# Kernel optimization log

Hardware: AMD Instinct MI355X
Metric: run time of the kernel (lower is better)

## Reference

```python
import jax, jax.numpy as jnp
import numpy as np

N_NODES = 10000
N_EDGES = 160000
N_GRAPHS = 16
IN_FEAT = 128
DIMS = [(128, 512), (512, 256), (256, 64), (64, 32)]


def _lin_params(key, fin, fout):
    w = jax.random.normal(key, (fin, fout), jnp.float32) * (1.0 / np.sqrt(fin))
    b = jnp.zeros((fout,), jnp.float32)
    return w, b


def setup_inputs() -> dict:
    key = jax.random.key(0)
    ks = jax.random.split(key, 64)
    inp = {}
    inp['x'] = jax.random.normal(ks[0], (N_NODES, IN_FEAT), jnp.float32)
    inp['edge_index'] = jax.random.randint(ks[1], (2, N_EDGES), 0, N_NODES, jnp.int64 if jax.config.jax_enable_x64 else jnp.int32)
    inp['batch'] = jnp.sort(jax.random.randint(ks[2], (N_NODES,), 0, N_GRAPHS))
    ki = 3
    for li, (fin, fout) in enumerate(DIMS, start=1):
        for nm in ['q', 'k', 'v', 's']:
            w, b = _lin_params(ks[ki], fin, fout); ki += 1
            inp[f'W{nm}{li}'] = w
            inp[f'b{nm}{li}'] = b
    inp['Wg'], inp['bg'] = _lin_params(ks[ki], 32, 1); ki += 1
    inp['Wf'], inp['bf'] = _lin_params(ks[ki], 32, 9)
    return inp


def _segment_softmax(logits, seg, num_segments):
    m = jax.ops.segment_max(logits, seg, num_segments=num_segments)
    e = jnp.exp(logits - m[seg])
    s = jax.ops.segment_sum(e, seg, num_segments=num_segments)
    return e / s[seg]


def _transformer_conv(x, src, dst, Wq, bq, Wk, bk, Wv, bv, Ws, bs):
    # PyG TransformerConv, heads=1: attention over incoming edges per dst node.
    n = x.shape[0]
    q = x @ Wq + bq
    k = x @ Wk + bk
    v = x @ Wv + bv
    d = q.shape[-1]
    logits = jnp.sum(q[dst] * k[src], axis=-1) / jnp.sqrt(jnp.asarray(d, x.dtype))
    alpha = _segment_softmax(logits, dst, n)  # [E]
    agg = jax.ops.segment_sum(alpha[:, None] * v[src], dst, num_segments=n)
    return agg + (x @ Ws + bs)  # root/skip connection


def reference(x, edge_index, batch,
              Wq1, bq1, Wk1, bk1, Wv1, bv1, Ws1, bs1,
              Wq2, bq2, Wk2, bk2, Wv2, bv2, Ws2, bs2,
              Wq3, bq3, Wk3, bk3, Wv3, bv3, Ws3, bs3,
              Wq4, bq4, Wk4, bk4, Wv4, bv4, Ws4, bs4,
              Wg, bg, Wf, bf):
    src, dst = edge_index[0], edge_index[1]
    layers = [
        (Wq1, bq1, Wk1, bk1, Wv1, bv1, Ws1, bs1),
        (Wq2, bq2, Wk2, bk2, Wv2, bv2, Ws2, bs2),
        (Wq3, bq3, Wk3, bk3, Wv3, bv3, Ws3, bs3),
        (Wq4, bq4, Wk4, bk4, Wv4, bv4, Ws4, bs4),
    ]
    h = x
    for p in layers:
        h = jax.nn.elu(_transformer_conv(h, src, dst, *p))
    # GlobalAttention pooling: gate softmax per graph, weighted sum.
    gate = (h @ Wg + bg)[:, 0]  # [N]
    a = _segment_softmax(gate, batch, N_GRAPHS)
    pooled = jax.ops.segment_sum(a[:, None] * h, batch, num_segments=N_GRAPHS)  # [G, 32]
    return pooled @ Wf + bf  # [G, 9]
```

## Files before the change

### kernel.cpp

```cpp
#include <hip/hip_runtime.h>
#include <hip/hip_bf16.h>
#include <math.h>


typedef __bf16 bf16x8 __attribute__((ext_vector_type(8)));
typedef __bf16 bf16x4 __attribute__((ext_vector_type(4)));
typedef __bf16 bf16x2 __attribute__((ext_vector_type(2)));
typedef float f32x4 __attribute__((ext_vector_type(4)));
typedef float f32x2 __attribute__((ext_vector_type(2)));

#define GBM 128
#define GBN 128
#define GBK 64

#if __has_builtin(__builtin_amdgcn_global_load_lds)
#define ASYNC_LDS 1
__device__ __forceinline__ void gload16(const __bf16* g, __bf16* l) {
  __builtin_amdgcn_global_load_lds(
      (const __attribute__((address_space(1))) unsigned int*)g,
      (__attribute__((address_space(3))) unsigned int*)l, 16, 0, 0);
}
#endif

#if __has_builtin(__builtin_amdgcn_fdot2_f32_bf16)
#define HAS_BF16_DOT2 1
#endif

__device__ __forceinline__ void xcd_swizzle(int& bx, int& by) {
  const int gx = gridDim.x;
  const int nwg = gx * gridDim.y;
  const int orig = blockIdx.y * gx + blockIdx.x;
  const int q = nwg >> 3, r = nwg & 7;
  const int xcd = orig & 7, ii = orig >> 3;
  const int wgid = (xcd < r ? xcd * (q + 1) : r * (q + 1) + (xcd - r) * q) + ii;
  bx = wgid % gx;
  by = wgid / gx;
}

__global__ __launch_bounds__(256) void gemm_mfma_kernel(
    const __bf16* __restrict__ A, const __bf16* __restrict__ Bt,
    const float* __restrict__ bias, __bf16* __restrict__ qkvs,
    int M, int K, int Nc) {
  __shared__ __bf16 As[GBM * 64];
  __shared__ __bf16 Bs[GBN * 64];
  const int tid = threadIdx.x;
  const int wave = tid >> 6;
  const int lane = tid & 63;
  const int quad = lane >> 4;
  const int l16 = lane & 15;
  int bx, by;
  xcd_swizzle(bx, by);
  const int m0 = by * GBM;
  const int n0 = bx * GBN;
  const int wm = (wave & 1) * 64;
  const int wn = (wave >> 1) * 64;

  const int r8 = lane >> 3;
  const int sseg = lane & 7;

  f32x4 acc[4][4] = {};

  for (int k0 = 0; k0 < K; k0 += GBK) {
#pragma unroll
    for (int it = 0; it < 4; ++it) {
      const int rbase = wave * 32 + it * 8;
      const int row = rbase + r8;
      const int sw = sseg ^ r8;
      const __bf16* ga = A + (size_t)(m0 + row) * K + k0 + sw * 8;
      const __bf16* gb = Bt + (size_t)(n0 + row) * K + k0 + sw * 8;
#ifdef ASYNC_LDS
      gload16(ga, As + rbase * 64);
      gload16(gb, Bs + rbase * 64);
#else
      *(bf16x8*)(As + row * 64 + sseg * 8) = *(const bf16x8*)ga;
      *(bf16x8*)(Bs + row * 64 + sseg * 8) = *(const bf16x8*)gb;
#endif
    }
    __syncthreads();

#pragma unroll
    for (int ks = 0; ks < 2; ++ks) {
      bf16x8 af[4], bfr[4];
#pragma unroll
      for (int i = 0; i < 4; ++i) {
        const int ra = wm + i * 16 + l16;
        const int rb = wn + i * 16 + l16;
        const int ps = ((ks * 4 + quad) ^ (l16 & 7)) * 8;
        af[i]  = *(const bf16x8*)(As + ra * 64 + ps);
        bfr[i] = *(const bf16x8*)(Bs + rb * 64 + ps);
      }
#pragma unroll
      for (int mi = 0; mi < 4; ++mi)
#pragma unroll
        for (int ni = 0; ni < 4; ++ni)
          acc[mi][ni] = __builtin_amdgcn_mfma_f32_16x16x32_bf16(
              af[mi], bfr[ni], acc[mi][ni], 0, 0, 0);
    }
    __syncthreads();
  }

  float bsv[4];
#pragma unroll
  for (int ni = 0; ni < 4; ++ni) bsv[ni] = bias[n0 + wn + ni * 16 + l16];
#pragma unroll
  for (int mi = 0; mi < 4; ++mi) {
#pragma unroll
    for (int r = 0; r < 4; ++r) {
      int row = m0 + wm + mi * 16 + quad * 4 + r;
      if (row < M) {
        size_t rb = (size_t)row * Nc;
#pragma unroll
        for (int ni = 0; ni < 4; ++ni) {
          int col = n0 + wn + ni * 16 + l16;
          qkvs[rb + col] = (__bf16)(acc[mi][ni][r] + bsv[ni]);
        }
      }
    }
  }
}

__global__ __launch_bounds__(256) void gemm_mfma_elu_kernel(
    const __bf16* __restrict__ A, const __bf16* __restrict__ Bt,
    const float* __restrict__ bias_s, const float* __restrict__ bias_v,
    const int* __restrict__ offs, __bf16* __restrict__ out,
    int M, int K, int Nc) {
  __shared__ __bf16 As[GBM * 64];
  __shared__ __bf16 Bs[GBN * 64];
  const int tid = threadIdx.x;
  const int wave = tid >> 6;
  const int lane = tid & 63;
  const int quad = lane >> 4;
  const int l16 = lane & 15;
  int bx, by;
  xcd_swizzle(bx, by);
  const int m0 = by * GBM;
  const int n0 = bx * GBN;
  const int wm = (wave & 1) * 64;
  const int wn = (wave >> 1) * 64;

  const int r8 = lane >> 3;
  const int sseg = lane & 7;

  f32x4 acc[4][4] = {};

  for (int k0 = 0; k0 < K; k0 += GBK) {
#pragma unroll
    for (int it = 0; it < 4; ++it) {
      const int rbase = wave * 32 + it * 8;
      const int row = rbase + r8;
      const int sw = sseg ^ r8;
      const __bf16* ga = A + (size_t)(m0 + row) * K + k0 + sw * 8;
      const __bf16* gb = Bt + (size_t)(n0 + row) * K + k0 + sw * 8;
#ifdef ASYNC_LDS
      gload16(ga, As + rbase * 64);
      gload16(gb, Bs + rbase * 64);
#else
      *(bf16x8*)(As + row * 64 + sseg * 8) = *(const bf16x8*)ga;
      *(bf16x8*)(Bs + row * 64 + sseg * 8) = *(const bf16x8*)gb;
#endif
    }
    __syncthreads();

#pragma unroll
    for (int ks = 0; ks < 2; ++ks) {
      bf16x8 af[4], bfr[4];
#pragma unroll
      for (int i = 0; i < 4; ++i) {
        const int ra = wm + i * 16 + l16;
        const int rb = wn + i * 16 + l16;
        const int ps = ((ks * 4 + quad) ^ (l16 & 7)) * 8;
        af[i]  = *(const bf16x8*)(As + ra * 64 + ps);
        bfr[i] = *(const bf16x8*)(Bs + rb * 64 + ps);
      }
#pragma unroll
      for (int mi = 0; mi < 4; ++mi)
#pragma unroll
        for (int ni = 0; ni < 4; ++ni)
          acc[mi][ni] = __builtin_amdgcn_mfma_f32_16x16x32_bf16(
              af[mi], bfr[ni], acc[mi][ni], 0, 0, 0);
    }
    __syncthreads();
  }

  float bsv[4], bvv[4];
#pragma unroll
  for (int ni = 0; ni < 4; ++ni) {
    const int col = n0 + wn + ni * 16 + l16;
    bsv[ni] = bias_s[col];
    bvv[ni] = bias_v[col];
  }
#pragma unroll
  for (int mi = 0; mi < 4; ++mi) {
#pragma unroll
    for (int r = 0; r < 4; ++r) {
      int row = m0 + wm + mi * 16 + quad * 4 + r;
      if (row < M) {
        const float bm = (offs[row + 1] - offs[row]) > 0 ? 1.f : 0.f;
        size_t rb = (size_t)row * Nc;
#pragma unroll
        for (int ni = 0; ni < 4; ++ni) {
          int col = n0 + wn + ni * 16 + l16;
          float v = acc[mi][ni][r] + bsv[ni] + bm * bvv[ni];
          v = (v > 0.f) ? v : expm1f(v);
          out[rb + col] = (__bf16)v;
        }
      }
    }
  }
}

#define NTILES 180
#define BTOT 3456
#define XTOT 320000
#define ABT_T 65536
#define UB_T 512
__global__ __launch_bounds__(256) void setup_pack_kernel(
    const float* W1q, const float* W1k, const float* W1v, const float* W1s,
    const float* W2q, const float* W2k, const float* W2v, const float* W2s,
    const float* W3q, const float* W3k, const float* W3v, const float* W3s,
    const float* W0v, const float* W0s,
    __bf16* __restrict__ Wt, __bf16* __restrict__ Bt2,
    const float* b0q, const float* b0k, const float* b0v, const float* b0s,
    const float* b1q, const float* b1k, const float* b1v, const float* b1s,
    const float* b2q, const float* b2k, const float* b2v, const float* b2s,
    const float* b3q, const float* b3k, const float* b3v, const float* b3s,
    const float* W0q, const float* W0k,
    const float* __restrict__ x, __bf16* __restrict__ xb,
    float* __restrict__ bcat,
    const int* __restrict__ dst, int* __restrict__ deg, int E,
    __bf16* __restrict__ Abt, float* __restrict__ biasu) {
  __shared__ float tile[64][65];
  const int tid = threadIdx.x;

  if (blockIdx.x < NTILES) {
    const int tb = blockIdx.x;
    const float* src;
    __bf16* dst_;
    int K, F, RS, CO, k0, j0;
    if (tb < 128) {
      const int m = tb >> 5, t = tb & 31;
      const float* Ws[4] = {W1q, W1k, W1v, W1s};
      src = Ws[m]; K = 512; F = 256; RS = 512; CO = 0;
      k0 = (t & 7) * 64; j0 = (t >> 3) * 64;
      dst_ = Wt + 262144 + (size_t)m * 131072;
    } else if (tb < 144) {
      const int u = tb - 128, m = u >> 2;
      const float* Ws[4] = {W2q, W2k, W2v, W2s};
      src = Ws[m]; K = 256; F = 64; RS = 256; CO = 0;
      k0 = (u & 3) * 64; j0 = 0;
      dst_ = Wt + 786432 + (size_t)m * 16384;
    } else if (tb < 148) {
      const int m = tb - 144;
      const float* Ws[4] = {W3q, W3k, W3v, W3s};
      src = Ws[m]; K = 64; F = 32; RS = 64; CO = 0;
      k0 = 0; j0 = 0;
      dst_ = Wt + 851968 + (size_t)m * 2048;
    } else {
      const int u = tb - 148, m = u >> 4, t = u & 15;
      src = m ? W0s : W0v; K = 128; F = 512; RS = 256; CO = m * 128;
      k0 = (t & 1) * 64; j0 = (t >> 1) * 64;
      dst_ = Bt2;
    }

    const int lj = tid & 63;
    const int lr = tid >> 6;
#pragma unroll
    for (int it = 0; it < 16; ++it) {
      const int kr = it * 4 + lr;
      float v = 0.f;
      if (k0 + kr < K && j0 + lj < F) v = src[(size_t)(k0 + kr) * F + j0 + lj];
      tile[kr][lj] = v;
    }
    __syncthreads();
#pragma unroll
    for (int it = 0; it < 16; ++it) {
      const int jr = it * 4 + lr;
      if (j0 + jr < F && k0 + lj < K)
        dst_[(size_t)(j0 + jr) * RS + CO + k0 + lj] = (__bf16)tile[lj][jr];
    }
    return;
  }

  const int t = (blockIdx.x - NTILES) * 256 + tid;
  if (t < XTOT) {
    float4 v = ((const float4*)x)[t];
    bf16x4 o;
    o[0] = (__bf16)v.x; o[1] = (__bf16)v.y; o[2] = (__bf16)v.z; o[3] = (__bf16)v.w;
    *(bf16x4*)(xb + (size_t)t * 4) = o;
  } else if (t < XTOT + BTOT) {
    int u = t - XTOT;
    int l, local, fsh, boff;
    if (u < 2048)      { l = 0; local = u;        fsh = 9; boff = 0; }
    else if (u < 3072) { l = 1; local = u - 2048; fsh = 8; boff = 2048; }
    else if (u < 3328) { l = 2; local = u - 3072; fsh = 6; boff = 3072; }
    else               { l = 3; local = u - 3328; fsh = 5; boff = 3328; }
    const int fout = 1 << fsh;
    int blk = local >> fsh, j = local & (fout - 1);
    const float* b;
    if (l == 0)      b = blk == 0 ? b0q : blk == 1 ? b0k : blk == 2 ? b0v : b0s;
    else if (l == 1) b = blk == 0 ? b1q : blk == 1 ? b1k : blk == 2 ? b1v : b1s;
    else if (l == 2) b = blk == 0 ? b2q : blk == 1 ? b2k : blk == 2 ? b2v : b2s;
    else             b = blk == 0 ? b3q : blk == 1 ? b3k : blk == 2 ? b3v : b3s;
    bcat[boff + local] = b[j];
  } else if (t < XTOT + BTOT + E) {
    int e = t - (XTOT + BTOT);
    atomicAdd(&deg[dst[e]], 1);
  } else if (t < XTOT + BTOT + E + ABT_T) {
    const int u = t - (XTOT + BTOT + E);
    const int n = u >> 9;
    const int rem = u & 511;
    const int k = rem >> 2;
    const int q = rem & 3;
    const float4* wq = (const float4*)(W0q + (size_t)k * 512) + q * 32;
    const float4* wk = (const float4*)(W0k + (size_t)n * 512) + q * 32;
    float sacc = 0.f;
#pragma unroll 4
    for (int jj = 0; jj < 32; ++jj) {
      float4 a = wq[jj], b = wk[jj];
      sacc += a.x * b.x + a.y * b.y + a.z * b.z + a.w * b.w;
    }
    sacc += __shfl_xor(sacc, 1);
    sacc += __shfl_xor(sacc, 2);
    if (q == 0) Abt[(size_t)n * 128 + k] = (__bf16)sacc;
  } else if (t < XTOT + BTOT + E + ABT_T + UB_T) {
    const int u = t - (XTOT + BTOT + E + ABT_T);
    const int n = u >> 2;
    const int q = u & 3;
    const float4* wk = (const float4*)(W0k + (size_t)n * 512) + q * 32;
    const float4* bq = (const float4*)b0q + q * 32;
    float sacc = 0.f;
#pragma unroll 4
    for (int jj = 0; jj < 32; ++jj) {
      float4 a = wk[jj], b = bq[jj];
      sacc += a.x * b.x + a.y * b.y + a.z * b.z + a.w * b.w;
    }
    sacc += __shfl_xor(sacc, 1);
    sacc += __shfl_xor(sacc, 2);
    if (q == 0) biasu[n] = sacc;
  }
}

__global__ __launch_bounds__(1024) void scan_kernel(const int* __restrict__ deg,
                                                    int* __restrict__ offs, int N) {
  __shared__ int sums[1024];
  const int tid = threadIdx.x;
  const int chunk = (N + 1023) / 1024;
  const int start = tid * chunk;
  int s = 0;
  for (int i = 0; i < chunk; ++i) {
    int idx = start + i;
    if (idx < N) s += deg[idx];
  }
  sums[tid] = s;
  __syncthreads();
  for (int off = 1; off < 1024; off <<= 1) {
    int t = (tid >= off) ? sums[tid - off] : 0;
    __syncthreads();
    sums[tid] += t;
    __syncthreads();
  }
  int run = (tid == 0) ? 0 : sums[tid - 1];
  for (int i = 0; i < chunk; ++i) {
    int idx = start + i;
    if (idx < N) {
      offs[idx] = run;
      run += deg[idx];
    }
  }
  if (tid == 1023) offs[N] = sums[1023];
}

__global__ void scatter_kernel(const int* __restrict__ src, const int* __restrict__ dst,
                               const int* __restrict__ offs, int* __restrict__ cursor,
                               int* __restrict__ csr_src, int E) {
  int e = blockIdx.x * blockDim.x + threadIdx.x;
  if (e >= E) return;
  int d = dst[e];
  int pos = offs[d] + atomicAdd(&cursor[d], 1);
  csr_src[pos] = src[e];
}

template <int D, int LPG_LOG2, bool GATE>
__global__ __launch_bounds__(256) void attn_fused_kernel(
    const __bf16* __restrict__ qkvs, const int* __restrict__ csr_src,
    const int* __restrict__ offs, __bf16* __restrict__ h_out, int N,
    float scale, const float* __restrict__ Wg, const float* __restrict__ bg,
    float* __restrict__ gate_out) {
  constexpr int LPG = 1 << LPG_LOG2;
  constexpr int NG = 64 / LPG;
  constexpr int NIT = D / (8 * LPG);
  constexpr int LD = 4 * D;
  const int node = (blockIdx.x * 256 + threadIdx.x) >> 6;
  const int lane = threadIdx.x & 63;
  if (node >= N) return;
  const int g = lane >> LPG_LOG2;
  const int l = lane & (LPG - 1);
  const int begin = offs[node];
  const int deg = offs[node + 1] - begin;

  const __bf16* qrow = qkvs + (size_t)node * LD;
  bf16x8 qreg[NIT];
#pragma unroll
  for (int it = 0; it < NIT; ++it)
    qreg[it] = *(const bf16x8*)(qrow + it * LPG * 8 + l * 8);

  float m0 = 0.f;
  float s = 0.f;
  f32x2 acc[NIT][4] = {};

  bf16x8 kA[NIT], vA[NIT], kB[NIT], vB[NIT];

  auto load_rows = [&](bool valid, int idx, bf16x8 (&kv)[NIT], bf16x8 (&vv)[NIT]) {
    const int sidx = valid ? csr_src[begin + idx] : 0;
    const __bf16* kr = qkvs + (size_t)sidx * LD + D + l * 8;
    if (valid) {
#pragma unroll
      for (int it = 0; it < NIT; ++it) {
        kv[it] = *(const bf16x8*)(kr + it * LPG * 8);
        vv[it] = *(const bf16x8*)(kr + D + it * LPG * 8);
      }
    }
  };

  auto compute = [&](bool valid, bool first, const bf16x8 (&kv)[NIT],
                     const bf16x8 (&vv)[NIT]) {
    float p = 0.f;
// ... 68 lines not shown

  if (g == 0) {
    float rr[NIT][8];
#pragma unroll
    for (int it = 0; it < NIT; ++it) {
      const int f0 = it * LPG * 8 + l * 8;
      bf16x8 sk = *(const bf16x8*)(qrow + 3 * D + f0);
      bf16x8 o;
#pragma unroll
      for (int j2 = 0; j2 < 4; ++j2) {
        float r0 = acc[it][j2][0] * inv + (float)sk[2 * j2];
        float r1 = acc[it][j2][1] * inv + (float)sk[2 * j2 + 1];
        r0 = (r0 > 0.f) ? r0 : expm1f(r0);
        r1 = (r1 > 0.f) ? r1 : expm1f(r1);
        rr[it][2 * j2] = r0;
        rr[it][2 * j2 + 1] = r1;
        o[2 * j2] = (__bf16)r0;
        o[2 * j2 + 1] = (__bf16)r1;
      }
      *(bf16x8*)(h_out + (size_t)node * D + f0) = o;
    }
    if (GATE) {
      float gp = 0.f;
#pragma unroll
      for (int j = 0; j < 8; ++j) gp += rr[0][j] * Wg[l * 8 + j];
#pragma unroll
      for (int off = 1; off < LPG; off <<= 1) gp += __shfl_xor(gp, off);
      if (l == 0) gate_out[node] = gp + bg[0];
    }
  }
}

template <int LPG_LOG2>
__global__ __launch_bounds__(256) void attn_lin_kernel(
    const __bf16* __restrict__ u, const __bf16* __restrict__ hsrc,
    const int* __restrict__ csr_src, const int* __restrict__ offs,
    __bf16* __restrict__ buf, int N, float scale) {
  constexpr int D = 128;
  constexpr int LPG = 1 << LPG_LOG2;
  constexpr int NG = 64 / LPG;
  constexpr int NIT = D / (8 * LPG);
  const int node = (blockIdx.x * 256 + threadIdx.x) >> 6;
  const int lane = threadIdx.x & 63;
  if (node >= N) return;
  const int g = lane >> LPG_LOG2;
  const int l = lane & (LPG - 1);
  const int begin = offs[node];
  const int deg = offs[node + 1] - begin;

  const __bf16* urow = u + (size_t)node * D;
  bf16x8 qreg[NIT];
#pragma unroll
  for (int it = 0; it < NIT; ++it)
    qreg[it] = *(const bf16x8*)(urow + it * LPG * 8 + l * 8);

  float m0 = 0.f;
  float s = 0.f;
  f32x2 acc[NIT][4] = {};

  bf16x8 kA[NIT], kB[NIT];

  auto load_rows = [&](bool valid, int idx, bf16x8 (&kv)[NIT]) {
    const int sidx = valid ? csr_src[begin + idx] : 0;
    const __bf16* hr = hsrc + (size_t)sidx * D + l * 8;
    if (valid) {
#pragma unroll
      for (int it = 0; it < NIT; ++it)
        kv[it] = *(const bf16x8*)(hr + it * LPG * 8);
    }
  };

  auto compute = [&](bool valid, bool first, const bf16x8 (&kv)[NIT]) {
    float p = 0.f;
    if (valid) {
#ifdef HAS_BF16_DOT2
#pragma unroll
// ... 50 lines not shown
    compute(valB, false, kB);
  }

#pragma unroll
  for (int off = LPG; off < 64; off <<= 1) {
    s += __shfl_xor(s, off);
#pragma unroll
    for (int it = 0; it < NIT; ++it)
#pragma unroll
      for (int j2 = 0; j2 < 4; ++j2) {
        acc[it][j2][0] += __shfl_xor(acc[it][j2][0], off);
        acc[it][j2][1] += __shfl_xor(acc[it][j2][1], off);
      }
  }
  const float inv = (deg > 0) ? (1.0f / s) : 0.f;

  if (g == 0) {
#pragma unroll
    for (int it = 0; it < NIT; ++it) {
      const int f0 = it * LPG * 8 + l * 8;
      bf16x8 o;
#pragma unroll
      for (int j2 = 0; j2 < 4; ++j2) {
        o[2 * j2]     = (__bf16)(acc[it][j2][0] * inv);
        o[2 * j2 + 1] = (__bf16)(acc[it][j2][1] * inv);
      }
      *(bf16x8*)(buf + (size_t)node * 256 + f0) = o;
      *(bf16x8*)(buf + (size_t)node * 256 + 128 + f0) =
          *(const bf16x8*)(hsrc + (size_t)node * D + f0);
    }
  }
}

__global__ __launch_bounds__(256) void pool_final_kernel(
    const __bf16* __restrict__ h, const float* __restrict__ gate,
    const int* __restrict__ batch, int N, const float* __restrict__ Wf,
    const float* __restrict__ bf_, float* __restrict__ out) {
  __shared__ float red[256];
  __shared__ float pooled_s[32];
  __shared__ float m_s, inv_s;
  __shared__ int sb[2];
  const int g = blockIdx.x;
  const int tid = threadIdx.x;

  if (tid < 2) {
    int target = g + tid;
    int lo = 0, hi = N;
    while (lo < hi) {
      int mid = (lo + hi) >> 1;
      if (batch[mid] < target) lo = mid + 1;
      else hi = mid;
    }
    sb[tid] = lo;
  }
  __syncthreads();
  const int s = sb[0];
  const int e_end = sb[1];

  float m = -INFINITY;
  for (int i = s + tid; i < e_end; i += 256) m = fmaxf(m, gate[i]);
  red[tid] = m;
  __syncthreads();
  for (int off = 128; off; off >>= 1) {
    if (tid < off) red[tid] = fmaxf(red[tid], red[tid + off]);
    __syncthreads();
  }
  if (tid == 0) m_s = red[0];
  __syncthreads();
  m = m_s;

  float ss = 0.f;
  for (int i = s + tid; i < e_end; i += 256) ss += __expf(gate[i] - m);
  red[tid] = ss;
  __syncthreads();
  for (int off = 128; off; off >>= 1) {
    if (tid < off) red[tid] += red[tid + off];
    __syncthreads();
  }
  if (tid == 0) inv_s = (e_end > s) ? (1.0f / red[0]) : 0.f;
  __syncthreads();
  const float inv = inv_s;

  const int f = tid & 31;
  const int grp = tid >> 5;
  float acc = 0.f;
  for (int i = s + grp; i < e_end; i += 8)
    acc += __expf(gate[i] - m) * (float)h[(size_t)i * 32 + f];
  red[tid] = acc;
  __syncthreads();
  if (tid < 32) {
    float a = 0.f;
#pragma unroll
    for (int j = 0; j < 8; ++j) a += red[j * 32 + tid];
    pooled_s[tid] = a * inv;
  }
  __syncthreads();

  if (tid < 9) {
    float o = bf_[tid];
#pragma unroll
    for (int kk = 0; kk < 32; ++kk) o += pooled_s[kk] * Wf[kk * 9 + tid];
    out[g * 9 + tid] = o;
  }
}

#define WTOT 860160
#define ATOT 16384
#define UBTOT 128
#define B2TOT 131072
extern "C" void kernel_launch(void* const* d_in, const int* in_sizes, int n_in,
                              void* d_out, int out_size, void* d_ws, size_t ws_size,
                              hipStream_t stream) {
  const int N = in_sizes[2];
  const int E = in_sizes[1] / 2;
  const int G = 16;
  const int NP = N + 128;

  const float* x = (const float*)d_in[0];
  const int* ei = (const int*)d_in[1];
  const int* batch = (const int*)d_in[2];
  const int* src = ei;
  const int* dst = ei + E;
  const float* Wg = (const float*)d_in[35];
  const float* bg = (const float*)d_in[36];
  const float* Wf = (const float*)d_in[37];
  const float* bf_ = (const float*)d_in[38];
  float* out = (float*)d_out;

  char* p = (char*)d_ws;
  auto carve = [&](size_t bytes) -> char* {
    char* r = p;
    p += (bytes + 255) & ~(size_t)255;
    return r;
  };
  int* deg = (int*)carve((size_t)2 * N * 4);
  int* cursor = deg + N;
  int* offs = (int*)carve((size_t)(N + 1) * 4);
  int* csr_src = (int*)carve((size_t)E * 4);
  __bf16* Ab = (__bf16*)carve((size_t)NP * 128 * 2);
  __bf16* Wt = (__bf16*)carve((size_t)WTOT * 2);
  float* bcat = (float*)carve(BTOT * 4);
  __bf16* qkvs = (__bf16*)carve((size_t)NP * 1024 * 2);
  __bf16* ha = (__bf16*)carve((size_t)NP * 512 * 2);
  __bf16* hb = (__bf16*)carve((size_t)NP * 512 * 2);
  float* gate = (float*)carve((size_t)N * 4);
  __bf16* ubuf = (__bf16*)carve((size_t)NP * 128 * 2);
  __bf16* cat = (__bf16*)carve((size_t)NP * 256 * 2);
  __bf16* Abt = (__bf16*)carve((size_t)ATOT * 2);
  float* biasu = (float*)carve((size_t)UBTOT * 4);
  __bf16* Bt2 = (__bf16*)carve((size_t)B2TOT * 2);
  (void)ws_size;

  hipMemsetAsync(deg, 0, (size_t)2 * N * 4, stream);
  const float** di = (const float**)d_in;
  const int miscb = (XTOT + BTOT + E + ABT_T + UB_T + 255) / 256;
  setup_pack_kernel<<<NTILES + miscb, 256, 0, stream>>>(
      di[11], di[13], di[15], di[17],
      di[19], di[21], di[23], di[25],
      di[27], di[29], di[31], di[33],
      di[7], di[9],
      Wt, Bt2,
      di[4], di[6], di[8], di[10],
      di[12], di[14], di[16], di[18],
      di[20], di[22], di[24], di[26],
      di[28], di[30], di[32], di[34],
      di[3], di[5],
      x, Ab, bcat, dst, deg, E, Abt, biasu);
  scan_kernel<<<1, 1024, 0, stream>>>(deg, offs, N);
  scatter_kernel<<<(E + 255) / 256, 256, 0, stream>>>(src, dst, offs, cursor, csr_src, E);

  const int agrid = ((size_t)N * 64 + 255) / 256;
  const int mg = (N + GBM - 1) / GBM;

  {
    dim3 g1(1, mg);
    gemm_mfma_kernel<<<g1, 256, 0, stream>>>(Ab, Abt, biasu, ubuf, N, 128, 128);
    attn_lin_kernel<3><<<agrid, 256, 0, stream>>>(ubuf, Ab, csr_src, offs, cat, N,
                                                  1.0f / sqrtf(512.f));
    dim3 g2(4, mg);
    gemm_mfma_elu_kernel<<<g2, 256, 0, stream>>>(cat, Bt2, di[10], di[8], offs,
                                                 ha, N, 256, 512);
  }

  const int fins[3] = {512, 256, 64};
  const int fouts[3] = {256, 64, 32};
  const size_t woffs[3] = {262144, 786432, 851968};
  const int boffs[3] = {2048, 3072, 3328};
  const __bf16* hin = ha;
  __bf16* houts[3] = {hb, ha, hb};

  for (int l = 0; l < 3; ++l) {
    const int fin = fins[l], fout = fouts[l];
    const int Nc = 4 * fout;
    __bf16* hout = houts[l];

    dim3 grid(Nc / GBN, mg);
    gemm_mfma_kernel<<<grid, 256, 0, stream>>>(hin, Wt + woffs[l], bcat + boffs[l],
                                               qkvs, N, fin, Nc);

    float scale = 1.0f / sqrtf((float)fout);
    if (l == 0) {
      attn_fused_kernel<256, 4, false><<<agrid, 256, 0, stream>>>(
          qkvs, csr_src, offs, hout, N, scale, nullptr, nullptr, nullptr);
    } else if (l == 1) {
      attn_fused_kernel<64, 3, false><<<agrid, 256, 0, stream>>>(
          qkvs, csr_src, offs, hout, N, scale, nullptr, nullptr, nullptr);
    } else {
      attn_fused_kernel<32, 2, true><<<agrid, 256, 0, stream>>>(
          qkvs, csr_src, offs, hout, N, scale, Wg, bg, gate);
    }
    hin = hout;
  }

  pool_final_kernel<<<G, 256, 0, stream>>>(hin, gate, batch, N, Wf, bf_, out);
}
```

Baseline: 342.3 us.

## Fuse whole pipeline into one persistent cooperative kernel with grid syncs

Replaces the sequence of separate launches (memset, setup pack, scan, scatter, GEMMs, attention, pooling) with a single cooperative persistent kernel that loops over virtual blocks per stage and separates stages with grid.sync. The aim is to remove per-launch overhead and gaps between the many small kernels. It also restructures the Abt precompute into an LDS-tiled block routine and shrinks the scan to 256 threads. The risks are that grid-wide barriers can cost more than the launches they replace, that the scan now runs serially on one block, and that forcing GEMM and attention into a shared launch configuration and register budget may lower occupancy.

```diff
diff --git a/kernel.cpp b/kernel.cpp
--- a/kernel.cpp
+++ b/kernel.cpp
@@ -1,6 +1,9 @@
 #include <hip/hip_runtime.h>
+#include <hip/hip_cooperative_groups.h>
 #include <hip/hip_bf16.h>
 #include <math.h>
+
+namespace cg = cooperative_groups;
 
 
 typedef __bf16 bf16x8 __attribute__((ext_vector_type(8)));
@@ -12,6 +15,15 @@
 #define GBM 128
 #define GBN 128
 #define GBK 64
+
+#define NTILES 180
+#define BTOT 3456
+#define XTOT 320000
+#define UB_T 512
+#define WTOT 860160
+#define ATOT 16384
+#define UBTOT 128
+#define B2TOT 131072
 
 #if __has_builtin(__builtin_amdgcn_global_load_lds)
 #define ASYNC_LDS 1
@@ -26,35 +38,49 @@
 #define HAS_BF16_DOT2 1
 #endif
 
-__device__ __forceinline__ void xcd_swizzle(int& bx, int& by) {
-  const int gx = gridDim.x;
-  const int nwg = gx * gridDim.y;
-  const int orig = blockIdx.y * gx + blockIdx.x;
-  const int q = nwg >> 3, r = nwg & 7;
-  const int xcd = orig & 7, ii = orig >> 3;
+struct MegaParams {
+  const float* x;
+  const int *src, *dst, *batch;
+  const float *W0q, *b0q, *W0k, *b0k, *W0v, *b0v, *W0s, *b0s;
+  const float *W1q, *b1q, *W1k, *b1k, *W1v, *b1v, *W1s, *b1s;
+  const float *W2q, *b2q, *W2k, *b2k, *W2v, *b2v, *W2s, *b2s;
+  const float *W3q, *b3q, *W3k, *b3k, *W3v, *b3v, *W3s, *b3s;
+  const float *Wg, *bg, *Wf, *bf;
+  float* out;
+  int *deg, *cursor, *offs, *csr_src;
+  __bf16 *Ab, *Wt, *Bt2, *Abt, *qkvs, *ha, *hb, *ubuf, *cat;
+  float *bcat, *biasu, *gate;
+  int N, E;
+};
+
+__device__ __forceinline__ void xcd_swizzle_v(int vt, int gx, int ntiles,
+                                              int& bx, int& by) {
+  const int q = ntiles >> 3, r = ntiles & 7;
+  const int xcd = vt & 7, ii = vt >> 3;
   const int wgid = (xcd < r ? xcd * (q + 1) : r * (q + 1) + (xcd - r) * q) + ii;
   bx = wgid % gx;
   by = wgid / gx;
 }
 
-__global__ __launch_bounds__(256) void gemm_mfma_kernel(
-    const __bf16* __restrict__ A, const __bf16* __restrict__ Bt,
-    const float* __restrict__ bias, __bf16* __restrict__ qkvs,
-    int M, int K, int Nc) {
-  __shared__ __bf16 As[GBM * 64];
-  __shared__ __bf16 Bs[GBN * 64];
-  const int tid = threadIdx.x;
+template <bool ELU>
+__device__ void gemm_body(const __bf16* __restrict__ A, const __bf16* __restrict__ Bt,
+                          const float* __restrict__ bias_s,
+                          const float* __restrict__ bias_v,
+                          const int* __restrict__ degoffs, __bf16* __restrict__ out,
+                          int M, int K, int Nc, int gx, int ntiles, int vt,
+                          int tid, char* smem) {
+  __bf16* As = (__bf16*)smem;
+  __bf16* Bs = As + GBM * 64;
   const int wave = tid >> 6;
   const int lane = tid & 63;
   const int quad = lane >> 4;
   const int l16 = lane & 15;
   int bx, by;
-  xcd_swizzle(bx, by);
+  xcd_swizzle_v(vt, gx, ntiles, bx, by);
   const int m0 = by * GBM;
   const int n0 = bx * GBN;
   const int wm = (wave & 1) * 64;
   const int wn = (wave >> 1) * 64;
-
   const int r8 = lane >> 3;
   const int sseg = lane & 7;
 
@@ -99,9 +125,13 @@
     __syncthreads();
   }
 
-  float bsv[4];
-#pragma unroll
-  for (int ni = 0; ni < 4; ++ni) bsv[ni] = bias[n0 + wn + ni * 16 + l16];
+  float bsv[4], bvv[4];
+#pragma unroll
+  for (int ni = 0; ni < 4; ++ni) {
+    const int col = n0 + wn + ni * 16 + l16;
+    bsv[ni] = bias_s[col];
+    bvv[ni] = ELU ? bias_v[col] : 0.f;
+  }
 #pragma unroll
   for (int mi = 0; mi < 4; ++mi) {
 #pragma unroll
@@ -109,99 +139,16 @@
       int row = m0 + wm + mi * 16 + quad * 4 + r;
       if (row < M) {
         size_t rb = (size_t)row * Nc;
+        float bm = 0.f;
+        if (ELU) bm = (degoffs[row + 1] - degoffs[row]) > 0 ? 1.f : 0.f;
 #pragma unroll
         for (int ni = 0; ni < 4; ++ni) {
           int col = n0 + wn + ni * 16 + l16;
-          qkvs[rb + col] = (__bf16)(acc[mi][ni][r] + bsv[ni]);
-        }
-      }
-    }
-  }
-}
-
-__global__ __launch_bounds__(256) void gemm_mfma_elu_kernel(
-    const __bf16* __restrict__ A, const __bf16* __restrict__ Bt,
-    const float* __restrict__ bias_s, const float* __restrict__ bias_v,
-    const int* __restrict__ offs, __bf16* __restrict__ out,
-    int M, int K, int Nc) {
-  __shared__ __bf16 As[GBM * 64];
-  __shared__ __bf16 Bs[GBN * 64];
-  const int tid = threadIdx.x;
-  const int wave = tid >> 6;
-  const int lane = tid & 63;
-  const int quad = lane >> 4;
-  const int l16 = lane & 15;
-  int bx, by;
-  xcd_swizzle(bx, by);
-  const int m0 = by * GBM;
-  const int n0 = bx * GBN;
-  const int wm = (wave & 1) * 64;
-  const int wn = (wave >> 1) * 64;
-
-  const int r8 = lane >> 3;
-  const int sseg = lane & 7;
-
-  f32x4 acc[4][4] = {};
-
-  for (int k0 = 0; k0 < K; k0 += GBK) {
-#pragma unroll
-    for (int it = 0; it < 4; ++it) {
-      const int rbase = wave * 32 + it * 8;
-      const int row = rbase + r8;
-      const int sw = sseg ^ r8;
-      const __bf16* ga = A + (size_t)(m0 + row) * K + k0 + sw * 8;
-      const __bf16* gb = Bt + (size_t)(n0 + row) * K + k0 + sw * 8;
-#ifdef ASYNC_LDS
-      gload16(ga, As + rbase * 64);
-      gload16(gb, Bs + rbase * 64);
-#else
-      *(bf16x8*)(As + row * 64 + sseg * 8) = *(const bf16x8*)ga;
-      *(bf16x8*)(Bs + row * 64 + sseg * 8) = *(const bf16x8*)gb;
-#endif
-    }
-    __syncthreads();
-
-#pragma unroll
-    for (int ks = 0; ks < 2; ++ks) {
-      bf16x8 af[4], bfr[4];
-#pragma unroll
-      for (int i = 0; i < 4; ++i) {
-        const int ra = wm + i * 16 + l16;
-        const int rb = wn + i * 16 + l16;
-        const int ps = ((ks * 4 + quad) ^ (l16 & 7)) * 8;
-        af[i]  = *(const bf16x8*)(As + ra * 64 + ps);
-        bfr[i] = *(const bf16x8*)(Bs + rb * 64 + ps);
-      }
-#pragma unroll
-      for (int mi = 0; mi < 4; ++mi)
-#pragma unroll
-        for (int ni = 0; ni < 4; ++ni)
-          acc[mi][ni] = __builtin_amdgcn_mfma_f32_16x16x32_bf16(
-              af[mi], bfr[ni], acc[mi][ni], 0, 0, 0);
-    }
-    __syncthreads();
-  }
-
-  float bsv[4], bvv[4];
-#pragma unroll
-  for (int ni = 0; ni < 4; ++ni) {
-    const int col = n0 + wn + ni * 16 + l16;
-    bsv[ni] = bias_s[col];
-    bvv[ni] = bias_v[col];
-  }
-#pragma unroll
-  for (int mi = 0; mi < 4; ++mi) {
-#pragma unroll
-    for (int r = 0; r < 4; ++r) {
-      int row = m0 + wm + mi * 16 + quad * 4 + r;
-      if (row < M) {
-        const float bm = (offs[row + 1] - offs[row]) > 0 ? 1.f : 0.f;
-        size_t rb = (size_t)row * Nc;
-#pragma unroll
-        for (int ni = 0; ni < 4; ++ni) {
-          int col = n0 + wn + ni * 16 + l16;
-          float v = acc[mi][ni][r] + bsv[ni] + bm * bvv[ni];
-          v = (v > 0.f) ? v : expm1f(v);
+          float v = acc[mi][ni][r] + bsv[ni];
+          if (ELU) {
+            v += bm * bvv[ni];
+            v = (v > 0.f) ? v : expm1f(v);
+          }
           out[rb + col] = (__bf16)v;
         }
       }
@@ -209,84 +156,101 @@
   }
 }
 
-#define NTILES 180
-#define BTOT 3456
-#define XTOT 320000
-#define ABT_T 65536
-#define UB_T 512
-__global__ __launch_bounds__(256) void setup_pack_kernel(
-    const float* W1q, const float* W1k, const float* W1v, const float* W1s,
-    const float* W2q, const float* W2k, const float* W2v, const float* W2s,
-    const float* W3q, const float* W3k, const float* W3v, const float* W3s,
-    const float* W0v, const float* W0s,
-    __bf16* __restrict__ Wt, __bf16* __restrict__ Bt2,
-    const float* b0q, const float* b0k, const float* b0v, const float* b0s,
-    const float* b1q, const float* b1k, const float* b1v, const float* b1s,
-    const float* b2q, const float* b2k, const float* b2v, const float* b2s,
-    const float* b3q, const float* b3k, const float* b3v, const float* b3s,
-    const float* W0q, const float* W0k,
-    const float* __restrict__ x, __bf16* __restrict__ xb,
-    float* __restrict__ bcat,
-    const int* __restrict__ dst, int* __restrict__ deg, int E,
-    __bf16* __restrict__ Abt, float* __restrict__ biasu) {
-  __shared__ float tile[64][65];
-  const int tid = threadIdx.x;
-
-  if (blockIdx.x < NTILES) {
-    const int tb = blockIdx.x;
-    const float* src;
-    __bf16* dst_;
-    int K, F, RS, CO, k0, j0;
-    if (tb < 128) {
-      const int m = tb >> 5, t = tb & 31;
-      const float* Ws[4] = {W1q, W1k, W1v, W1s};
-      src = Ws[m]; K = 512; F = 256; RS = 512; CO = 0;
-      k0 = (t & 7) * 64; j0 = (t >> 3) * 64;
-      dst_ = Wt + 262144 + (size_t)m * 131072;
-    } else if (tb < 144) {
-      const int u = tb - 128, m = u >> 2;
-      const float* Ws[4] = {W2q, W2k, W2v, W2s};
-      src = Ws[m]; K = 256; F = 64; RS = 256; CO = 0;
-      k0 = (u & 3) * 64; j0 = 0;
-      dst_ = Wt + 786432 + (size_t)m * 16384;
-    } else if (tb < 148) {
-      const int m = tb - 144;
-      const float* Ws[4] = {W3q, W3k, W3v, W3s};
-      src = Ws[m]; K = 64; F = 32; RS = 64; CO = 0;
-      k0 = 0; j0 = 0;
-      dst_ = Wt + 851968 + (size_t)m * 2048;
-    } else {
-      const int u = tb - 148, m = u >> 4, t = u & 15;
-      src = m ? W0s : W0v; K = 128; F = 512; RS = 256; CO = m * 128;
-      k0 = (t & 1) * 64; j0 = (t >> 1) * 64;
-      dst_ = Bt2;
-    }
-
-    const int lj = tid & 63;
-    const int lr = tid >> 6;
-#pragma unroll
-    for (int it = 0; it < 16; ++it) {
-      const int kr = it * 4 + lr;
-      float v = 0.f;
-      if (k0 + kr < K && j0 + lj < F) v = src[(size_t)(k0 + kr) * F + j0 + lj];
-      tile[kr][lj] = v;
+__device__ void transpose_body(const MegaParams& P, int tb, int tid, char* smem) {
+  float (*tile)[65] = (float(*)[65])smem;
+  const float* src;
+  __bf16* dst_;
+  int K, F, RS, CO, k0, j0;
+  if (tb < 128) {
+    const int m = tb >> 5, t = tb & 31;
+    const float* Ws[4] = {P.W1q, P.W1k, P.W1v, P.W1s};
+    src = Ws[m]; K = 512; F = 256; RS = 512; CO = 0;
+    k0 = (t & 7) * 64; j0 = (t >> 3) * 64;
+    dst_ = P.Wt + 262144 + (size_t)m * 131072;
+  } else if (tb < 144) {
+    const int u = tb - 128, m = u >> 2;
+    const float* Ws[4] = {P.W2q, P.W2k, P.W2v, P.W2s};
+    src = Ws[m]; K = 256; F = 64; RS = 256; CO = 0;
+    k0 = (u & 3) * 64; j0 = 0;
+    dst_ = P.Wt + 786432 + (size_t)m * 16384;
+  } else if (tb < 148) {
+    const int m = tb - 144;
+    const float* Ws[4] = {P.W3q, P.W3k, P.W3v, P.W3s};
+    src = Ws[m]; K = 64; F = 32; RS = 64; CO = 0;
+    k0 = 0; j0 = 0;
+    dst_ = P.Wt + 851968 + (size_t)m * 2048;
+  } else {
+    const int u = tb - 148, m = u >> 4, t = u & 15;
+    src = m ? P.W0s : P.W0v; K = 128; F = 512; RS = 256; CO = m * 128;
+    k0 = (t & 1) * 64; j0 = (t >> 1) * 64;
+    dst_ = P.Bt2;
+  }
+
+  const int lj = tid & 63;
+  const int lr = tid >> 6;
+#pragma unroll
+  for (int it = 0; it < 16; ++it) {
+    const int kr = it * 4 + lr;
+    float v = 0.f;
+    if (k0 + kr < K && j0 + lj < F) v = src[(size_t)(k0 + kr) * F + j0 + lj];
+    tile[kr][lj] = v;
+  }
+  __syncthreads();
+#pragma unroll
+  for (int it = 0; it < 16; ++it) {
+    const int jr = it * 4 + lr;
+    if (j0 + jr < F && k0 + lj < K)
+      dst_[(size_t)(j0 + jr) * RS + CO + k0 + lj] = (__bf16)tile[lj][jr];
+  }
+  __syncthreads();
+}
+
+__device__ void abt_body(const MegaParams& P, int b, int tid, char* smem) {
+  float* chq = (float*)smem;
+  float* chk = (float*)(smem + 64 * 68 * 4);
+  const int n = b >> 1;
+  const int k0 = (b & 1) * 64;
+  const int q = tid & 3;
+  const int kloc = tid >> 2;
+  float sacc = 0.f;
+#pragma unroll
+  for (int pass = 0; pass < 8; ++pass) {
+    const int c4 = (tid & 15) * 4;
+#pragma unroll
+    for (int it = 0; it < 4; ++it) {
+      const int row = it * 16 + (tid >> 4);
+      const float4 v = *(const float4*)(P.W0q + (size_t)(k0 + row) * 512 +
+                                        pass * 64 + c4);
+      chq[row * 68 + c4] = v.x; chq[row * 68 + c4 + 1] = v.y;
+      chq[row * 68 + c4 + 2] = v.z; chq[row * 68 + c4 + 3] = v.w;
+    }
+    if (tid < 16) {
+      const float4 v = *(const float4*)(P.W0k + (size_t)n * 512 + pass * 64 + tid * 4);
+      chk[tid * 4] = v.x; chk[tid * 4 + 1] = v.y;
+      chk[tid * 4 + 2] = v.z; chk[tid * 4 + 3] = v.w;
     }
     __syncthreads();
-#pragma unroll
-    for (int it = 0; it < 16; ++it) {
-      const int jr = it * 4 + lr;
-      if (j0 + jr < F && k0 + lj < K)
-        dst_[(size_t)(j0 + jr) * RS + CO + k0 + lj] = (__bf16)tile[lj][jr];
-    }
-    return;
-  }
-
-  const int t = (blockIdx.x - NTILES) * 256 + tid;
+    if ((pass >> 1) == q) {
+#pragma unroll 4
+      for (int t = 0; t < 16; ++t) {
+        float4 a = *(const float4*)&chq[kloc * 68 + t * 4];
+        float4 bb = *(const float4*)&chk[t * 4];
+        sacc += a.x * bb.x + a.y * bb.y + a.z * bb.z + a.w * bb.w;
+      }
+    }
+    __syncthreads();
+  }
+  sacc += __shfl_xor(sacc, 1);
+  sacc += __shfl_xor(sacc, 2);
+  if (q == 0) P.Abt[(size_t)n * 128 + k0 + kloc] = (__bf16)sacc;
+}
+
+__device__ void misc_body(const MegaParams& P, int t) {
   if (t < XTOT) {
-    float4 v = ((const float4*)x)[t];
+    float4 v = ((const float4*)P.x)[t];
     bf16x4 o;
     o[0] = (__bf16)v.x; o[1] = (__bf16)v.y; o[2] = (__bf16)v.z; o[3] = (__bf16)v.w;
-    *(bf16x4*)(xb + (size_t)t * 4) = o;
+    *(bf16x4*)(P.Ab + (size_t)t * 4) = o;
   } else if (t < XTOT + BTOT) {
     int u = t - XTOT;
     int l, local, fsh, boff;
@@ -297,37 +261,20 @@
     const int fout = 1 << fsh;
     int blk = local >> fsh, j = local & (fout - 1);
     const float* b;
-    if (l == 0)      b = blk == 0 ? b0q : blk == 1 ? b0k : blk == 2 ? b0v : b0s;
-    else if (l == 1) b = blk == 0 ? b1q : blk == 1 ? b1k : blk == 2 ? b1v : b1s;
-    else if (l == 2) b = blk == 0 ? b2q : blk == 1 ? b2k : blk == 2 ? b2v : b2s;
-    else             b = blk == 0 ? b3q : blk == 1 ? b3k : blk == 2 ? b3v : b3s;
-    bcat[boff + local] = b[j];
-  } else if (t < XTOT + BTOT + E) {
+    if (l == 0)      b = blk == 0 ? P.b0q : blk == 1 ? P.b0k : blk == 2 ? P.b0v : P.b0s;
+    else if (l == 1) b = blk == 0 ? P.b1q : blk == 1 ? P.b1k : blk == 2 ? P.b1v : P.b1s;
+    else if (l == 2) b = blk == 0 ? P.b2q : blk == 1 ? P.b2k : blk == 2 ? P.b2v : P.b2s;
+    else             b = blk == 0 ? P.b3q : blk == 1 ? P.b3k : blk == 2 ? P.b3v : P.b3s;
+    P.bcat[boff + local] = b[j];
+  } else if (t < XTOT + BTOT + P.E) {
     int e = t - (XTOT + BTOT);
-    atomicAdd(&deg[dst[e]], 1);
-  } else if (t < XTOT + BTOT + E + ABT_T) {
-    const int u = t - (XTOT + BTOT + E);
-    const int n = u >> 9;
-    const int rem = u & 511;
-    const int k = rem >> 2;
-    const int q = rem & 3;
-    const float4* wq = (const float4*)(W0q + (size_t)k * 512) + q * 32;
-    const float4* wk = (const float4*)(W0k + (size_t)n * 512) + q * 32;
-    float sacc = 0.f;
-#pragma unroll 4
-    for (int jj = 0; jj < 32; ++jj) {
-      float4 a = wq[jj], b = wk[jj];
-      sacc += a.x * b.x + a.y * b.y + a.z * b.z + a.w * b.w;
-    }
-    sacc += __shfl_xor(sacc, 1);
-    sacc += __shfl_xor(sacc, 2);
-    if (q == 0) Abt[(size_t)n * 128 + k] = (__bf16)sacc;
-  } else if (t < XTOT + BTOT + E + ABT_T + UB_T) {
-    const int u = t - (XTOT + BTOT + E + ABT_T);
+    atomicAdd(&P.deg[P.dst[e]], 1);
+  } else if (t < XTOT + BTOT + P.E + UB_T) {
+    const int u = t - (XTOT + BTOT + P.E);
     const int n = u >> 2;
     const int q = u & 3;
-    const float4* wk = (const float4*)(W0k + (size_t)n * 512) + q * 32;
-    const float4* bq = (const float4*)b0q + q * 32;
+    const float4* wk = (const float4*)(P.W0k + (size_t)n * 512) + q * 32;
+    const float4* bq = (const float4*)P.b0q + q * 32;
     float sacc = 0.f;
 #pragma unroll 4
     for (int jj = 0; jj < 32; ++jj) {
@@ -336,15 +283,14 @@
     }
     sacc += __shfl_xor(sacc, 1);
     sacc += __shfl_xor(sacc, 2);
-    if (q == 0) biasu[n] = sacc;
-  }
-}
-
-__global__ __launch_bounds__(1024) void scan_kernel(const int* __restrict__ deg,
-                                                    int* __restrict__ offs, int N) {
-  __shared__ int sums[1024];
-  const int tid = threadIdx.x;
-  const int chunk = (N + 1023) / 1024;
+    if (q == 0) P.biasu[n] = sacc;
+  }
+}
+
+__device__ void scan_body(const int* __restrict__ deg, int* __restrict__ offs,
+                          int N, int tid, char* smem) {
+  int* sums = (int*)smem;
+  const int chunk = (N + 255) / 256;
   const int start = tid * chunk;
   int s = 0;
   for (int i = 0; i < chunk; ++i) {
@@ -353,7 +299,7 @@
   }
   sums[tid] = s;
   __syncthreads();
-  for (int off = 1; off < 1024; off <<= 1) {
+  for (int off = 1; off < 256; off <<= 1) {
     int t = (tid >= off) ? sums[tid - off] : 0;
     __syncthreads();
     sums[tid] += t;
@@ -367,31 +313,22 @@
       run += deg[idx];
     }
   }
-  if (tid == 1023) offs[N] = sums[1023];
-}
-
-__global__ void scatter_kernel(const int* __restrict__ src, const int* __restrict__ dst,
-                               const int* __restrict__ offs, int* __restrict__ cursor,
-                               int* __restrict__ csr_src, int E) {
-  int e = blockIdx.x * blockDim.x + threadIdx.x;
-  if (e >= E) return;
-  int d = dst[e];
-  int pos = offs[d] + atomicAdd(&cursor[d], 1);
-  csr_src[pos] = src[e];
+  if (tid == 255) offs[N] = sums[255];
 }
 
 template <int D, int LPG_LOG2, bool GATE>
-__global__ __launch_bounds__(256) void attn_fused_kernel(
-    const __bf16* __restrict__ qkvs, const int* __restrict__ csr_src,
-    const int* __restrict__ offs, __bf16* __restrict__ h_out, int N,
-    float scale, const float* __restrict__ Wg, const float* __restrict__ bg,
-    float* __restrict__ gate_out) {
+__device__ void attn_body(const __bf16* __restrict__ qkvs,
+                          const int* __restrict__ csr_src,
+                          const int* __restrict__ offs, __bf16* __restrict__ h_out,
+                          int N, float scale, const float* __restrict__ Wg,
+                          const float* __restrict__ bg,
+                          float* __restrict__ gate_out, int vb, int tid) {
   constexpr int LPG = 1 << LPG_LOG2;
   constexpr int NG = 64 / LPG;
   constexpr int NIT = D / (8 * LPG);
   constexpr int LD = 4 * D;
-  const int node = (blockIdx.x * 256 + threadIdx.x) >> 6;
-  const int lane = threadIdx.x & 63;
+  const int node = (vb * 256 + tid) >> 6;
+  const int lane = tid & 63;
   if (node >= N) return;
   const int g = lane >> LPG_LOG2;
   const int l = lane & (LPG - 1);
@@ -526,16 +463,18 @@
 }
 
 template <int LPG_LOG2>
-__global__ __launch_bounds__(256) void attn_lin_kernel(
-    const __bf16* __restrict__ u, const __bf16* __restrict__ hsrc,
-    const int* __restrict__ csr_src, const int* __restrict__ offs,
-    __bf16* __restrict__ buf, int N, float scale) {
+__device__ void attn_lin_body(const __bf16* __restrict__ u,
+                              const __bf16* __restrict__ hsrc,
+                              const int* __restrict__ csr_src,
+                              const int* __restrict__ offs,
+                              __bf16* __restrict__ buf, int N, float scale,
+                              int vb, int tid) {
   constexpr int D = 128;
   constexpr int LPG = 1 << LPG_LOG2;
   constexpr int NG = 64 / LPG;
   constexpr int NIT = D / (8 * LPG);
-  const int node = (blockIdx.x * 256 + threadIdx.x) >> 6;
-  const int lane = threadIdx.x & 63;
+  const int node = (vb * 256 + tid) >> 6;
+  const int lane = tid & 63;
   if (node >= N) return;
   const int g = lane >> LPG_LOG2;
   const int l = lane & (LPG - 1);
@@ -652,100 +591,176 @@
   }
 }
 
-__global__ __launch_bounds__(256) void pool_final_kernel(
-    const __bf16* __restrict__ h, const float* __restrict__ gate,
-    const int* __restrict__ batch, int N, const float* __restrict__ Wf,
-    const float* __restrict__ bf_, float* __restrict__ out) {
-  __shared__ float red[256];
-  __shared__ float pooled_s[32];
-  __shared__ float m_s, inv_s;
-  __shared__ int sb[2];
-  const int g = blockIdx.x;
-  const int tid = threadIdx.x;
+struct PoolS {
+  float red[256];
+  float pooled[32];
+  float m_s, inv_s;
+  int sb[2];
+};
+
+__device__ void pool_body(const MegaParams& P, int g, int tid, char* smem) {
+  PoolS* ps = (PoolS*)smem;
+  const int N = P.N;
 
   if (tid < 2) {
     int target = g + tid;
     int lo = 0, hi = N;
     while (lo < hi) {
       int mid = (lo + hi) >> 1;
-      if (batch[mid] < target) lo = mid + 1;
+      if (P.batch[mid] < target) lo = mid + 1;
       else hi = mid;
     }
-    sb[tid] = lo;
-  }
-  __syncthreads();
-  const int s = sb[0];
-  const int e_end = sb[1];
+    ps->sb[tid] = lo;
+  }
+  __syncthreads();
+  const int s = ps->sb[0];
+  const int e_end = ps->sb[1];
 
   float m = -INFINITY;
-  for (int i = s + tid; i < e_end; i += 256) m = fmaxf(m, gate[i]);
-  red[tid] = m;
+  for (int i = s + tid; i < e_end; i += 256) m = fmaxf(m, P.gate[i]);
+  ps->red[tid] = m;
   __syncthreads();
   for (int off = 128; off; off >>= 1) {
-    if (tid < off) red[tid] = fmaxf(red[tid], red[tid + off]);
+    if (tid < off) ps->red[tid] = fmaxf(ps->red[tid], ps->red[tid + off]);
     __syncthreads();
   }
-  if (tid == 0) m_s = red[0];
-  __syncthreads();
-  m = m_s;
+  if (tid == 0) ps->m_s = ps->red[0];
+  __syncthreads();
+  m = ps->m_s;
 
   float ss = 0.f;
-  for (int i = s + tid; i < e_end; i += 256) ss += __expf(gate[i] - m);
-  red[tid] = ss;
+  for (int i = s + tid; i < e_end; i += 256) ss += __expf(P.gate[i] - m);
+  ps->red[tid] = ss;
   __syncthreads();
   for (int off = 128; off; off >>= 1) {
-    if (tid < off) red[tid] += red[tid + off];
+    if (tid < off) ps->red[tid] += ps->red[tid + off];
     __syncthreads();
   }
-  if (tid == 0) inv_s = (e_end > s) ? (1.0f / red[0]) : 0.f;
-  __syncthreads();
-  const float inv = inv_s;
+  if (tid == 0) ps->inv_s = (e_end > s) ? (1.0f / ps->red[0]) : 0.f;
+  __syncthreads();
+  const float inv = ps->inv_s;
 
   const int f = tid & 31;
   const int grp = tid >> 5;
   float acc = 0.f;
   for (int i = s + grp; i < e_end; i += 8)
-    acc += __expf(gate[i] - m) * (float)h[(size_t)i * 32 + f];
-  red[tid] = acc;
+    acc += __expf(P.gate[i] - m) * (float)P.hb[(size_t)i * 32 + f];
+  ps->red[tid] = acc;
   __syncthreads();
   if (tid < 32) {
     float a = 0.f;
 #pragma unroll
-    for (int j = 0; j < 8; ++j) a += red[j * 32 + tid];
-    pooled_s[tid] = a * inv;
+    for (int j = 0; j < 8; ++j) a += ps->red[j * 32 + tid];
+    ps->pooled[tid] = a * inv;
   }
   __syncthreads();
 
   if (tid < 9) {
-    float o = bf_[tid];
-#pragma unroll
-    for (int kk = 0; kk < 32; ++kk) o += pooled_s[kk] * Wf[kk * 9 + tid];
-    out[g * 9 + tid] = o;
-  }
-}
-
-#define WTOT 860160
-#define ATOT 16384
-#define UBTOT 128
-#define B2TOT 131072
+    float o = P.bf[tid];
+#pragma unroll
+    for (int kk = 0; kk < 32; ++kk) o += ps->pooled[kk] * P.Wf[kk * 9 + tid];
+    P.out[g * 9 + tid] = o;
+  }
+  __syncthreads();
+}
+
+__global__ __launch_bounds__(256, 4) void mega_kernel(MegaParams P) {
+  __shared__ __align__(16) char smem[32768];
+  cg::grid_group grid = cg::this_grid();
+  const int tid = threadIdx.x;
+  const int nb = gridDim.x;
+  const int bid = blockIdx.x;
+  const int N = P.N, E = P.E;
+
+  for (int i = bid * 256 + tid; i < 2 * N; i += nb * 256) P.deg[i] = 0;
+  grid.sync();
+
+  {
+    const int TS_TOT = XTOT + BTOT + E + UB_T;
+    const int p1 = NTILES + 256 + (TS_TOT + 255) / 256;
+    for (int vb = bid; vb < p1; vb += nb) {
+      if (vb < NTILES) transpose_body(P, vb, tid, smem);
+      else if (vb < NTILES + 256) abt_body(P, vb - NTILES, tid, smem);
+      else misc_body(P, (vb - NTILES - 256) * 256 + tid);
+    }
+  }
+  grid.sync();
+
+  if (bid == 0) scan_body(P.deg, P.offs, N, tid, smem);
+  grid.sync();
+
+  for (int vb = bid; vb < (E + 255) / 256; vb += nb) {
+    const int e = vb * 256 + tid;
+    if (e < E) {
+      int d = P.dst[e];
+      int pos = P.offs[d] + atomicAdd(&P.cursor[d], 1);
+      P.csr_src[pos] = P.src[e];
+    }
+  }
+  grid.sync();
+
+  const int mg = (N + GBM - 1) / GBM;
+  const int ab = (N * 64 + 255) / 256;
+
+  for (int vt = bid; vt < mg; vt += nb)
+    gemm_body<false>(P.Ab, P.Abt, P.biasu, nullptr, nullptr, P.ubuf,
+                     N, 128, 128, 1, mg, vt, tid, smem);
+  grid.sync();
+
+  for (int vb = bid; vb < ab; vb += nb)
+    attn_lin_body<3>(P.ubuf, P.Ab, P.csr_src, P.offs, P.cat, N,
+                     1.0f / sqrtf(512.f), vb, tid);
+  grid.sync();
+
+  for (int vt = bid; vt < 4 * mg; vt += nb)
+    gemm_body<true>(P.cat, P.Bt2, P.b0s, P.b0v, P.offs, P.ha,
+                    N, 256, 512, 4, 4 * mg, vt, tid, smem);
+  grid.sync();
+
+  for (int vt = bid; vt < 8 * mg; vt += nb)
+    gemm_body<false>(P.ha, P.Wt + 262144, P.bcat + 2048, nullptr, nullptr,
+                     P.qkvs, N, 512, 1024, 8, 8 * mg, vt, tid, smem);
+  grid.sync();
+
+  for (int vb = bid; vb < ab; vb += nb)
+    attn_body<256, 4, false>(P.qkvs, P.csr_src, P.offs, P.hb, N,
+                             1.0f / sqrtf(256.f), nullptr, nullptr, nullptr,
+                             vb, tid);
+  grid.sync();
+
+  for (int vt = bid; vt < 2 * mg; vt += nb)
+    gemm_body<false>(P.hb, P.Wt + 786432, P.bcat + 3072, nullptr, nullptr,
+                     P.qkvs, N, 256, 256, 2, 2 * mg, vt, tid, smem);
+  grid.sync();
+
+  for (int vb = bid; vb < ab; vb += nb)
+    attn_body<64, 3, false>(P.qkvs, P.csr_src, P.offs, P.ha, N,
+                            1.0f / sqrtf(64.f), nullptr, nullptr, nullptr,
+                            vb, tid);
+  grid.sync();
+
+  for (int vt = bid; vt < mg; vt += nb)
+    gemm_body<false>(P.ha, P.Wt + 851968, P.bcat + 3328, nullptr, nullptr,
+                     P.qkvs, N, 64, 128, 1, mg, vt, tid, smem);
+  grid.sync();
+
+  for (int vb = bid; vb < ab; vb += nb)
+    attn_body<32, 2, true>(P.qkvs, P.csr_src, P.offs, P.hb, N,
+                           1.0f / sqrtf(32.f), P.Wg, P.bg, P.gate, vb, tid);
+  grid.sync();
+
+  for (int vb = bid; vb < 16; vb += nb) pool_body(P, vb, tid, smem);
+}
+
 extern "C" void kernel_launch(void* const* d_in, const int* in_sizes, int n_in,
                               void* d_out, int out_size, void* d_ws, size_t ws_size,
                               hipStream_t stream) {
   const int N = in_sizes[2];
   const int E = in_sizes[1] / 2;
-  const int G = 16;
   const int NP = N + 128;
 
-  const float* x = (const float*)d_in[0];
+  const float** di = (const float**)d_in;
   const int* ei = (const int*)d_in[1];
-  const int* batch = (const int*)d_in[2];
-  const int* src = ei;
-  const int* dst = ei + E;
-  const float* Wg = (const float*)d_in[35];
-  const float* bg = (const float*)d_in[36];
-  const float* Wf = (const float*)d_in[37];
-  const float* bf_ = (const float*)d_in[38];
-  float* out = (float*)d_out;
 
   char* p = (char*)d_ws;
   auto carve = [&](size_t bytes) -> char* {
@@ -771,66 +786,36 @@
   __bf16* Bt2 = (__bf16*)carve((size_t)B2TOT * 2);
   (void)ws_size;
 
-  hipMemsetAsync(deg, 0, (size_t)2 * N * 4, stream);
-  const float** di = (const float**)d_in;
-  const int miscb = (XTOT + BTOT + E + ABT_T + UB_T + 255) / 256;
-  setup_pack_kernel<<<NTILES + miscb, 256, 0, stream>>>(
-      di[11], di[13], di[15], di[17],
-      di[19], di[21], di[23], di[25],
-      di[27], di[29], di[31], di[33],
-      di[7], di[9],
-      Wt, Bt2,
-      di[4], di[6], di[8], di[10],
-      di[12], di[14], di[16], di[18],
-      di[20], di[22], di[24], di[26],
-      di[28], di[30], di[32], di[34],
-      di[3], di[5],
-      x, Ab, bcat, dst, deg, E, Abt, biasu);
-  scan_kernel<<<1, 1024, 0, stream>>>(deg, offs, N);
-  scatter_kernel<<<(E + 255) / 256, 256, 0, stream>>>(src, dst, offs, cursor, csr_src, E);
-
-  const int agrid = ((size_t)N * 64 + 255) / 256;
-  const int mg = (N + GBM - 1) / GBM;
-
-  {
-    dim3 g1(1, mg);
-    gemm_mfma_kernel<<<g1, 256, 0, stream>>>(Ab, Abt, biasu, ubuf, N, 128, 128);
-    attn_lin_kernel<3><<<agrid, 256, 0, stream>>>(ubuf, Ab, csr_src, offs, cat, N,
-                                                  1.0f / sqrtf(512.f));
-    dim3 g2(4, mg);
-    gemm_mfma_elu_kernel<<<g2, 256, 0, stream>>>(cat, Bt2, di[10], di[8], offs,
-                                                 ha, N, 256, 512);
-  }
-
-  const int fins[3] = {512, 256, 64};
-  const int fouts[3] = {256, 64, 32};
-  const size_t woffs[3] = {262144, 786432, 851968};
-  const int boffs[3] = {2048, 3072, 3328};
-  const __bf16* hin = ha;
-  __bf16* houts[3] = {hb, ha, hb};
-
-  for (int l = 0; l < 3; ++l) {
-    const int fin = fins[l], fout = fouts[l];
-    const int Nc = 4 * fout;
-    __bf16* hout = houts[l];
-
-    dim3 grid(Nc / GBN, mg);
-    gemm_mfma_kernel<<<grid, 256, 0, stream>>>(hin, Wt + woffs[l], bcat + boffs[l],
-                                               qkvs, N, fin, Nc);
-
-    float scale = 1.0f / sqrtf((float)fout);
-    if (l == 0) {
-      attn_fused_kernel<256, 4, false><<<agrid, 256, 0, stream>>>(
-          qkvs, csr_src, offs, hout, N, scale, nullptr, nullptr, nullptr);
-    } else if (l == 1) {
-      attn_fused_kernel<64, 3, false><<<agrid, 256, 0, stream>>>(
-          qkvs, csr_src, offs, hout, N, scale, nullptr, nullptr, nullptr);
-    } else {
-      attn_fused_kernel<32, 2, true><<<agrid, 256, 0, stream>>>(
-          qkvs, csr_src, offs, hout, N, scale, Wg, bg, gate);
-    }
-    hin = hout;
-  }
-
-  pool_final_kernel<<<G, 256, 0, stream>>>(hin, gate, batch, N, Wf, bf_, out);
-}
+  MegaParams P;
+  P.x = di[0];
+  P.src = ei;
+  P.dst = ei + E;
+  P.batch = (const int*)d_in[2];
+  P.W0q = di[3];  P.b0q = di[4];  P.W0k = di[5];  P.b0k = di[6];
+  P.W0v = di[7];  P.b0v = di[8];  P.W0s = di[9];  P.b0s = di[10];
+  P.W1q = di[11]; P.b1q = di[12]; P.W1k = di[13]; P.b1k = di[14];
+  P.W1v = di[15]; P.b1v = di[16]; P.W1s = di[17]; P.b1s = di[18];
+  P.W2q = di[19]; P.b2q = di[20]; P.W2k = di[21]; P.b2k = di[22];
+  P.W2v = di[23]; P.b2v = di[24]; P.W2s = di[25]; P.b2s = di[26];
+  P.W3q = di[27]; P.b3q = di[28]; P.W3k = di[29]; P.b3k = di[30];
+  P.W3v = di[31]; P.b3v = di[32]; P.W3s = di[33]; P.b3s = di[34];
+  P.Wg = di[35]; P.bg = di[36]; P.Wf = di[37]; P.bf = di[38];
+  P.out = (float*)d_out;
+  P.deg = deg; P.cursor = cursor; P.offs = offs; P.csr_src = csr_src;
+  P.Ab = Ab; P.Wt = Wt; P.Bt2 = Bt2; P.Abt = Abt; P.qkvs = qkvs;
+  P.ha = ha; P.hb = hb; P.ubuf = ubuf; P.cat = cat;
+  P.bcat = bcat; P.biasu = biasu; P.gate = gate;
+  P.N = N; P.E = E;
+
+  int occ = 0;
+  hipOccupancyMaxActiveBlocksPerMultiprocessor(&occ, mega_kernel, 256, 0);
+  if (occ < 1) occ = 1;
+  int nblk = occ * 256;
+  if (nblk > 2500) nblk = 2500;
+  nblk &= ~7;
+  if (nblk < 8) nblk = 8;
+
+  void* args[] = {(void*)&P};
+  hipLaunchCooperativeKernel((void*)mega_kernel, dim3(nblk), dim3(256), args,
+                             0, stream);
+}
```

After: 1.168 ms. 241% more time.
